# Kernel optimization log

Hardware: AMD Instinct MI355X
Metric: run time of the kernel (lower is better)

## Reference

```python
import jax, jax.numpy as jnp
import numpy as np

KH = KW = 3
STRIDE = 1
PAD = 1
IN_CH = 16
OUT_CH = 64


def unfold(x, kh, kw, pad, stride):
    """PyTorch F.unfold: (N,C,H,W) -> (N, C*kh*kw, L), channel slowest, then kh, kw."""
    x = jnp.pad(x, ((0, 0), (0, 0), (pad, pad), (pad, pad)))
    N, C, H, W = x.shape
    Ho = (H - kh) // stride + 1
    Wo = (W - kw) // stride + 1
    # stack the kh*kw shifted views: (N, C, kh*kw, Ho, Wo)
    patches = jnp.stack(
        [x[:, :, i:i + stride * Ho:stride, j:j + stride * Wo:stride]
         for i in range(kh) for j in range(kw)], axis=2)
    return patches.reshape(N, C * kh * kw, Ho * Wo)


def setup_inputs() -> dict:
    key = jax.random.key(0)
    k1, k2 = jax.random.split(key)
    x = jax.random.normal(k1, (8, IN_CH, 32, 32), dtype=jnp.float32)
    weight = jax.random.normal(k2, (OUT_CH, IN_CH * KH * KW), dtype=jnp.float32)  # std=1.0
    bias = jnp.zeros((OUT_CH,), dtype=jnp.float32)
    return {"x": x, "weight": weight, "bias": bias}


def reference(x, weight, bias):
    N, C, H, W = x.shape
    Ho = (H + 2 * PAD - KH) // STRIDE + 1
    Wo = (W + 2 * PAD - KW) // STRIDE + 1
    cols = unfold(x, KH, KW, PAD, STRIDE)              # (N, F, L)
    # L-inf distance between each patch column and each weight row:
    # out[n,o,l] = max_f |cols[n,f,l] - weight[o,f]|
    diff = jnp.abs(cols[:, None, :, :] - weight[None, :, :, None])  # (N, O, F, L)
    dist = jnp.max(diff, axis=2)                       # (N, O, L)
    out = dist + bias[None, :, None]
    return out.reshape(N, OUT_CH, Ho, Wo)
```

## Files before the change

kernel.cpp:

```cpp
#include <hip/hip_runtime.h>


#define N_ 8
#define C_ 16
#define H_ 32
#define W_ 32
#define O_ 64
#define F_ 144
#define HT 8
#define RT (HT + 2)
#define RSTR 36

__global__ __launch_bounds__(256)
void normdist_kernel(const float* __restrict__ x,
                     const float* __restrict__ weight,
                     const float* __restrict__ bias,
                     float* __restrict__ out)
{
    __shared__ float xs[C_ * RT * RSTR];
    __shared__ float sc[3][2][HT][W_];

    const int tid = threadIdx.x;
    const int o0  = blockIdx.x * 2;
    const int h0  = blockIdx.y * HT;
    const int n   = blockIdx.z;

    const float* __restrict__ xn = x + (size_t)n * (C_ * H_ * W_);
    const float* __restrict__ wr = weight + (size_t)o0 * F_;

    #pragma unroll
    for (int k = 0; k < 5; ++k) {
        int idx  = tid + k * 256;
        int swq  = idx & 7;
        int c    = (idx >> 3) & 15;
        int r    = idx >> 7;
        int grow = h0 - 1 + r;
        float4 v = make_float4(0.f, 0.f, 0.f, 0.f);
        if (grow >= 0 && grow < H_)
            v = *reinterpret_cast<const float4*>(xn + c * (H_ * W_) + grow * W_ + swq * 4);
        *reinterpret_cast<float4*>(&xs[(c * RT + r) * RSTR + swq * 4]) = v;
    }
    __syncthreads();

    const int wq = tid & 7;
    const int hl = (tid >> 3) & 7;
    const int g  = tid >> 6;
    const int w0 = wq * 4;
    const bool left_edge  = (wq == 0);
    const bool right_edge = (wq == 7);

    const int cbase = __builtin_amdgcn_readfirstlane(g) * 4;

    float m[2][4];
    #pragma unroll
    for (int og = 0; og < 2; ++og)
        #pragma unroll
        for (int p = 0; p < 4; ++p)
            m[og][p] = 0.f;

    #pragma unroll
    for (int cc = 0; cc < 4; ++cc) {
        const int c = cbase + cc;
        #pragma unroll
        for (int kh = 0; kh < 3; ++kh) {
            const int R = hl + kh;
            float4 xm = *reinterpret_cast<const float4*>(&xs[(c * RT + R) * RSTR + w0]);
            float xl = __shfl_up(xm.w, 1);
            float xr = __shfl_down(xm.x, 1);
            xl = left_edge  ? 0.f : xl;
            xr = right_edge ? 0.f : xr;
            float xw[6] = {xl, xm.x, xm.y, xm.z, xm.w, xr};
            const int f = c * 9 + kh * 3;
            #pragma unroll
            for (int og = 0; og < 2; ++og) {
                const float wv0 = wr[og * F_ + f + 0];
                const float wv1 = wr[og * F_ + f + 1];
                const float wv2 = wr[og * F_ + f + 2];
                #pragma unroll
                for (int p = 0; p < 4; ++p) {
                    float v0 = __builtin_fabsf(xw[p + 0] - wv0);
                    float v1 = __builtin_fabsf(xw[p + 1] - wv1);
                    float v2 = __builtin_fabsf(xw[p + 2] - wv2);
                    float mm = m[og][p];
                    mm = fmaxf(fmaxf(mm, v0), v1);
                    m[og][p] = fmaxf(mm, v2);
                }
            }
        }
    }

    if (g > 0) {
        #pragma unroll
        for (int og = 0; og < 2; ++og)
            *reinterpret_cast<float4*>(&sc[g - 1][og][hl][w0]) =
                make_float4(m[og][0], m[og][1], m[og][2], m[og][3]);
    }
    __syncthreads();

    if (g == 0) {
        #pragma unroll
        for (int og = 0; og < 2; ++og) {
            float4 a = *reinterpret_cast<const float4*>(&sc[0][og][hl][w0]);
            float4 b = *reinterpret_cast<const float4*>(&sc[1][og][hl][w0]);
            float4 d = *reinterpret_cast<const float4*>(&sc[2][og][hl][w0]);
            const float bv = bias[o0 + og];
            float4 r;
            r.x = fmaxf(fmaxf(fmaxf(m[og][0], a.x), b.x), d.x) + bv;
            r.y = fmaxf(fmaxf(fmaxf(m[og][1], a.y), b.y), d.y) + bv;
            r.z = fmaxf(fmaxf(fmaxf(m[og][2], a.z), b.z), d.z) + bv;
            r.w = fmaxf(fmaxf(fmaxf(m[og][3], a.w), b.w), d.w) + bv;
            float* dst = out + ((size_t)(n * O_ + o0 + og) * (H_ * W_))
                             + (h0 + hl) * W_ + w0;
            *reinterpret_cast<float4*>(dst) = r;
        }
    }
}

extern "C" void kernel_launch(void* const* d_in, const int* in_sizes, int n_in,
                              void* d_out, int out_size, void* d_ws, size_t ws_size,
                              hipStream_t stream) {
    const float* x  = (const float*)d_in[0];
    const float* w  = (const float*)d_in[1];
    const float* b  = (const float*)d_in[2];
    float* out      = (float*)d_out;

    dim3 grid(O_ / 2, H_ / HT, N_);
    dim3 block(256);
    hipLaunchKernelGGL(normdist_kernel, grid, block, 0, stream, x, w, b, out);
}
```

Before: 10.58 us.

## Remap work so each lane owns one output channel with weights held in registers

The kernel is reorganised so each block covers one output row and a 16-wide column strip, and each lane handles one of the 64 output channels. That lane's 72-element weight half sits in registers, and the input patch is staged in LDS, where all lanes of a wave read the same address as a broadcast. Two channel halves are reduced through LDS, replacing the old four-way split with per-iteration weight loads from global memory and shuffles. The cost is heavy register pressure, which may lower occupancy, and more blocks each doing less work. Output stores are now strided across channels, so writes are less coalesced.

```diff
diff --git a/kernel.cpp b/kernel.cpp
--- a/kernel.cpp
+++ b/kernel.cpp
@@ -7,112 +7,98 @@
 #define W_ 32
 #define O_ 64
 #define F_ 144
-#define HT 8
-#define RT (HT + 2)
-#define RSTR 36
 
-__global__ __launch_bounds__(256)
+typedef __attribute__((ext_vector_type(4))) float f4;
+
+__global__ __launch_bounds__(512, 4)
 void normdist_kernel(const float* __restrict__ x,
                      const float* __restrict__ weight,
                      const float* __restrict__ bias,
                      float* __restrict__ out)
 {
-    __shared__ float xs[C_ * RT * RSTR];
-    __shared__ float sc[3][2][HT][W_];
+    __shared__ float xs[C_ * 3 * 24];
+    __shared__ f4    sc[4][O_];
 
-    const int tid = threadIdx.x;
-    const int o0  = blockIdx.x * 2;
-    const int h0  = blockIdx.y * HT;
-    const int n   = blockIdx.z;
+    const int tid   = threadIdx.x;
+    const int h     = blockIdx.x;
+    const int wbase = blockIdx.y * 16;
+    const int n     = blockIdx.z;
 
     const float* __restrict__ xn = x + (size_t)n * (C_ * H_ * W_);
-    const float* __restrict__ wr = weight + (size_t)o0 * F_;
+
+    for (int t = tid; t < C_ * 3 * 18; t += 512) {
+        int wloc = t % 18;
+        int r    = (t / 18) % 3;
+        int c    = t / 54;
+        int gw   = wbase - 1 + wloc;
+        int gr   = h - 1 + r;
+        float v = 0.f;
+        if (gr >= 0 && gr < H_ && gw >= 0 && gw < W_)
+            v = xn[c * (H_ * W_) + gr * W_ + gw];
+        xs[(c * 3 + r) * 24 + 3 + wloc] = v;
+    }
+
+    const int lane = tid & 63;
+    const int wv64 = tid >> 6;
+    const int q    = wv64 & 3;
+    const int ch   = wv64 >> 2;
+
+    f4 wv[18];
+    const float* wrow = weight + (size_t)lane * F_ + ch * 72;
+    #pragma unroll
+    for (int t = 0; t < 18; ++t)
+        wv[t] = *reinterpret_cast<const f4*>(wrow + 4 * t);
+
+    __syncthreads();
+
+    const float* xq = xs + ch * (8 * 3 * 24) + 4 * q;
+    float m0 = 0.f, m1 = 0.f, m2 = 0.f, m3 = 0.f;
 
     #pragma unroll
-    for (int k = 0; k < 5; ++k) {
-        int idx  = tid + k * 256;
-        int swq  = idx & 7;
-        int c    = (idx >> 3) & 15;
-        int r    = idx >> 7;
-        int grow = h0 - 1 + r;
-        float4 v = make_float4(0.f, 0.f, 0.f, 0.f);
-        if (grow >= 0 && grow < H_)
-            v = *reinterpret_cast<const float4*>(xn + c * (H_ * W_) + grow * W_ + swq * 4);
-        *reinterpret_cast<float4*>(&xs[(c * RT + r) * RSTR + swq * 4]) = v;
+    for (int cc = 0; cc < 8; ++cc) {
+        #pragma unroll
+        for (int kh = 0; kh < 3; ++kh) {
+            const float* rp = xq + cc * 72 + kh * 24;
+            float xw0 = rp[3];
+            f4    xm  = *reinterpret_cast<const f4*>(rp + 4);
+            float xw5 = rp[8];
+            float xw1 = xm[0], xw2 = xm[1], xw3 = xm[2], xw4 = xm[3];
+            const int j = cc * 9 + kh * 3;
+            float w0v = wv[(j + 0) >> 2][(j + 0) & 3];
+            float w1v = wv[(j + 1) >> 2][(j + 1) & 3];
+            float w2v = wv[(j + 2) >> 2][(j + 2) & 3];
+            m0 = fmaxf(fmaxf(fmaxf(m0, __builtin_fabsf(xw0 - w0v)),
+                             __builtin_fabsf(xw1 - w1v)),
+                       __builtin_fabsf(xw2 - w2v));
+            m1 = fmaxf(fmaxf(fmaxf(m1, __builtin_fabsf(xw1 - w0v)),
+                             __builtin_fabsf(xw2 - w1v)),
+                       __builtin_fabsf(xw3 - w2v));
+            m2 = fmaxf(fmaxf(fmaxf(m2, __builtin_fabsf(xw2 - w0v)),
+                             __builtin_fabsf(xw3 - w1v)),
+                       __builtin_fabsf(xw4 - w2v));
+            m3 = fmaxf(fmaxf(fmaxf(m3, __builtin_fabsf(xw3 - w0v)),
+                             __builtin_fabsf(xw4 - w1v)),
+                       __builtin_fabsf(xw5 - w2v));
+        }
+    }
+
+    if (ch == 1) {
+        f4 v; v[0] = m0; v[1] = m1; v[2] = m2; v[3] = m3;
+        sc[q][lane] = v;
     }
     __syncthreads();
 
-    const int wq = tid & 7;
-    const int hl = (tid >> 3) & 7;
-    const int g  = tid >> 6;
-    const int w0 = wq * 4;
-    const bool left_edge  = (wq == 0);
-    const bool right_edge = (wq == 7);
-
-    const int cbase = __builtin_amdgcn_readfirstlane(g) * 4;
-
-    float m[2][4];
-    #pragma unroll
-    for (int og = 0; og < 2; ++og)
-        #pragma unroll
-        for (int p = 0; p < 4; ++p)
-            m[og][p] = 0.f;
-
-    #pragma unroll
-    for (int cc = 0; cc < 4; ++cc) {
-        const int c = cbase + cc;
-        #pragma unroll
-        for (int kh = 0; kh < 3; ++kh) {
-            const int R = hl + kh;
-            float4 xm = *reinterpret_cast<const float4*>(&xs[(c * RT + R) * RSTR + w0]);
-            float xl = __shfl_up(xm.w, 1);
-            float xr = __shfl_down(xm.x, 1);
-            xl = left_edge  ? 0.f : xl;
-            xr = right_edge ? 0.f : xr;
-            float xw[6] = {xl, xm.x, xm.y, xm.z, xm.w, xr};
-            const int f = c * 9 + kh * 3;
-            #pragma unroll
-            for (int og = 0; og < 2; ++og) {
-                const float wv0 = wr[og * F_ + f + 0];
-                const float wv1 = wr[og * F_ + f + 1];
-                const float wv2 = wr[og * F_ + f + 2];
-                #pragma unroll
-                for (int p = 0; p < 4; ++p) {
-                    float v0 = __builtin_fabsf(xw[p + 0] - wv0);
-                    float v1 = __builtin_fabsf(xw[p + 1] - wv1);
-                    float v2 = __builtin_fabsf(xw[p + 2] - wv2);
-                    float mm = m[og][p];
-                    mm = fmaxf(fmaxf(mm, v0), v1);
-                    m[og][p] = fmaxf(mm, v2);
-                }
-            }
-        }
-    }
-
-    if (g > 0) {
-        #pragma unroll
-        for (int og = 0; og < 2; ++og)
-            *reinterpret_cast<float4*>(&sc[g - 1][og][hl][w0]) =
-                make_float4(m[og][0], m[og][1], m[og][2], m[og][3]);
-    }
-    __syncthreads();
-
-    if (g == 0) {
-        #pragma unroll
-        for (int og = 0; og < 2; ++og) {
-            float4 a = *reinterpret_cast<const float4*>(&sc[0][og][hl][w0]);
-            float4 b = *reinterpret_cast<const float4*>(&sc[1][og][hl][w0]);
-            float4 d = *reinterpret_cast<const float4*>(&sc[2][og][hl][w0]);
-            const float bv = bias[o0 + og];
-            float4 r;
-            r.x = fmaxf(fmaxf(fmaxf(m[og][0], a.x), b.x), d.x) + bv;
-            r.y = fmaxf(fmaxf(fmaxf(m[og][1], a.y), b.y), d.y) + bv;
-            r.z = fmaxf(fmaxf(fmaxf(m[og][2], a.z), b.z), d.z) + bv;
-            r.w = fmaxf(fmaxf(fmaxf(m[og][3], a.w), b.w), d.w) + bv;
-            float* dst = out + ((size_t)(n * O_ + o0 + og) * (H_ * W_))
-                             + (h0 + hl) * W_ + w0;
-            *reinterpret_cast<float4*>(dst) = r;
-        }
+    if (ch == 0) {
+        f4 p = sc[q][lane];
+        const float bv = bias[lane];
+        f4 r;
+        r[0] = fmaxf(m0, p[0]) + bv;
+        r[1] = fmaxf(m1, p[1]) + bv;
+        r[2] = fmaxf(m2, p[2]) + bv;
+        r[3] = fmaxf(m3, p[3]) + bv;
+        float* dst = out + ((size_t)(n * O_ + lane) * (H_ * W_))
+                         + h * W_ + wbase + 4 * q;
+        *reinterpret_cast<f4*>(dst) = r;
     }
 }
 
@@ -124,7 +110,7 @@
     const float* b  = (const float*)d_in[2];
     float* out      = (float*)d_out;
 
-    dim3 grid(O_ / 2, H_ / HT, N_);
-    dim3 block(256);
+    dim3 grid(H_, 2, N_);
+    dim3 block(512);
     hipLaunchKernelGGL(normdist_kernel, grid, block, 0, stream, x, w, b, out);
 }
```

Result: slower. 12.73 us (+20.3%).
